# Optimization experiments

Hardware: AMD Instinct MI355X
Metric: run time of the kernel (lower is better)

The kernel has to match this reference:

```python
import jax, jax.numpy as jnp
import numpy as np

EPS = 1e-8  # F.cosine_similarity default eps


def setup_inputs() -> dict:
    key = jax.random.key(0)
    k1, k2, k3, k4 = jax.random.split(key, 4)
    Q, P, E, V = 4096, 16384, 128, 30000
    query = jax.random.randint(k1, (Q,), 0, V, dtype=jnp.int64)
    para = jax.random.randint(k2, (P,), 0, V, dtype=jnp.int64)
    que_embed = jax.random.normal(k3, (Q, E), dtype=jnp.float32)
    para_embed = jax.random.normal(k4, (P, E), dtype=jnp.float32)
    return {"query": query, "para": para, "que_embed": que_embed, "para_embed": para_embed}


def reference(query, para, que_embed, para_embed):
    # xor_matrix[i, j] = 1 if query[i] == para[j] else 0  -> [Q, P] int64
    xor_matrix = (query[:, None] == para[None, :]).astype(jnp.int64)
    # cos_matrix[i, j] = cosine_similarity(que_embed[i], para_embed[j])
    # torch semantics: dot / (max(||q||, eps) * max(||p||, eps))
    q_norm = jnp.maximum(jnp.linalg.norm(que_embed, axis=-1), EPS)   # [Q]
    p_norm = jnp.maximum(jnp.linalg.norm(para_embed, axis=-1), EPS)  # [P]
    dots = jnp.einsum('qe,pe->qp', que_embed, para_embed)            # [Q, P]
    cos_matrix = dots / (q_norm[:, None] * p_norm[None, :])
    return xor_matrix, cos_matrix
```

## Files before the change

### kernel.cpp

```cpp
#include <hip/hip_runtime.h>
#include <stdint.h>

typedef __attribute__((ext_vector_type(8))) short bf16x8;
typedef __attribute__((ext_vector_type(4))) float f32x4;

__device__ __forceinline__ uint32_t f2bf(float f) {
    uint32_t u = __builtin_bit_cast(uint32_t, f);
    u += 0x7fffu + ((u >> 16) & 1u);
    return u >> 16;
}
__device__ __forceinline__ uint32_t pack2(float a, float b) {
    return f2bf(a) | (f2bf(b) << 16);
}

__global__ __launch_bounds__(256) void prep_norms(const float* __restrict__ qe,
                                                  const float* __restrict__ pe,
                                                  float* __restrict__ rq,
                                                  float* __restrict__ rp,
                                                  int Q, int Pn) {
    int gw = (blockIdx.x * 256 + threadIdx.x) >> 6;
    int lane = threadIdx.x & 63;
    if (gw >= Q + Pn) return;
    const float* src = (gw < Q) ? (qe + (size_t)gw * 128) : (pe + (size_t)(gw - Q) * 128);
    float2 v = *(const float2*)(src + lane * 2);
    float s = v.x * v.x + v.y * v.y;
#pragma unroll
    for (int off = 32; off > 0; off >>= 1) s += __shfl_down(s, off, 64);
    if (lane == 0) {
        float r = 1.0f / fmaxf(sqrtf(s), 1e-8f);
        if (gw < Q) rq[gw] = r; else rp[gw - Q] = r;
    }
}

__global__ __launch_bounds__(256) void conv_frag(const float* __restrict__ src,
                                                 unsigned short* __restrict__ dst,
                                                 int ngroups) {
    int t = blockIdx.x * 256 + threadIdx.x;
    if (t >= ngroups * 256) return;
    int g = t >> 8, rem = t & 255;
    int c = rem >> 6, lane = rem & 63;
    int row = g * 16 + (lane & 15);
    int col = c * 32 + ((lane >> 4) << 3);
    const float* s = src + (size_t)row * 128 + col;
    float4 a0 = *(const float4*)s;
    float4 a1 = *(const float4*)(s + 4);
    uint4 pk = { pack2(a0.x, a0.y), pack2(a0.z, a0.w),
                 pack2(a1.x, a1.y), pack2(a1.z, a1.w) };
    *(uint4*)(dst + (size_t)t * 8) = pk;
}

#define PBLK 2048

__global__ __launch_bounds__(256, 4) void fused_gemm(
        const unsigned short* __restrict__ Qf, const unsigned short* __restrict__ Pf,
        const int* __restrict__ qid, const int* __restrict__ pid,
        const float* __restrict__ rq, const float* __restrict__ rp,
        float* __restrict__ oxor, float* __restrict__ ocos, int Pn) {
    __shared__ __align__(16) float scos[4 * 16 * 65];

    const int nwg = gridDim.x;
    const int chunk = nwg >> 3;
    const int bid = blockIdx.x;
    const int wg = (bid & 7) * chunk + (bid >> 3);
    const int nPc = Pn / PBLK;
    const int qg = wg / nPc;
    const int pc = wg % nPc;
    const int pblock = pc * PBLK;

    const int t = threadIdx.x;
    const int lane = t & 63;
    const int w = t >> 6;
    const int lq = lane & 15;
    const int g4 = (lane >> 4) << 2;
    const int wbase = w * (16 * 65);

    bf16x8 af[4];
    const unsigned short* abase = Qf + ((size_t)(qg * 4) * 64 + lane) * 8;
#pragma unroll
    for (int kk = 0; kk < 4; ++kk)
        af[kk] = *(const bf16x8*)(abase + kk * 512);

    const int qrow_base = qg * 16;
    const float rqv = rq[qrow_base + lq];

    for (int fl = 0; fl < PBLK / 256; ++fl) {
        const int pw = pblock + fl * 256 + w * 64;
#pragma unroll
        for (int f = 0; f < 4; ++f) {
            const int p0 = pw + f * 16;
            const unsigned short* bbase = Pf + (size_t)(p0 >> 4) * 2048 + (size_t)lane * 8;
            bf16x8 bfr[4];
#pragma unroll
            for (int kk = 0; kk < 4; ++kk)
                bfr[kk] = *(const bf16x8*)(bbase + kk * 512);
            f32x4 acc = {0.f, 0.f, 0.f, 0.f};
#pragma unroll
            for (int kk = 0; kk < 4; ++kk)
                acc = __builtin_amdgcn_mfma_f32_16x16x32_bf16(bfr[kk], af[kk], acc, 0, 0, 0);
            const float4 rpv = *(const float4*)(rp + p0 + g4);
            const int a0 = wbase + lq * 65 + f * 16 + g4;
            scos[a0 + 0] = acc[0] * rqv * rpv.x;
            scos[a0 + 1] = acc[1] * rqv * rpv.y;
            scos[a0 + 2] = acc[2] * rqv * rpv.z;
            scos[a0 + 3] = acc[3] * rqv * rpv.w;
        }
        const int pvl = pid[pw + lane];
#pragma unroll
        for (int r = 0; r < 16; ++r) {
            const int qvr = qid[qrow_base + r];
            const size_t obase = (size_t)(qrow_base + r) * Pn + pw;
            float vc = scos[wbase + r * 65 + lane];
            float vx = (qvr == pvl) ? 1.f : 0.f;
            ocos[obase + lane] = vc;
            oxor[obase + lane] = vx;
        }
    }
}

extern "C" void kernel_launch(void* const* d_in, const int* in_sizes, int n_in,
                              void* d_out, int out_size, void* d_ws, size_t ws_size,
                              hipStream_t stream) {
    const int*   qid = (const int*)d_in[0];
    const int*   pid = (const int*)d_in[1];
    const float* qe  = (const float*)d_in[2];
    const float* pe  = (const float*)d_in[3];
    const int Q  = in_sizes[0];
    const int Pn = in_sizes[1];

    unsigned short* Qf = (unsigned short*)d_ws;
    unsigned short* Pf = Qf + (size_t)Q * 128;
    float* rq = (float*)(Pf + (size_t)Pn * 128);
    float* rp = rq + Q;

    float* oxor = (float*)d_out;
    float* ocos = oxor + (size_t)Q * (size_t)Pn;

    const int qgroups = Q / 16, pgroups = Pn / 16;
    conv_frag<<<qgroups, 256, 0, stream>>>(qe, Qf, qgroups);
    conv_frag<<<pgroups, 256, 0, stream>>>(pe, Pf, pgroups);
    prep_norms<<<(Q + Pn + 3) / 4, 256, 0, stream>>>(qe, pe, rq, rp, Q, Pn);

    const int nblocks = (Q / 16) * (Pn / PBLK);
    fused_gemm<<<nblocks, 256, 0, stream>>>(Qf, Pf, qid, pid, rq, rp, oxor, ocos, Pn);
}
```

Measured before the change: 138.0 us.

## Split xor output into separate streaming kernel and vectorize cos stores

Moves the xor-matrix generation out of the GEMM into a dedicated streaming kernel that writes four floats per thread with nontemporal stores. The GEMM epilogue now writes only the cosine matrix, using 16-byte vector LDS reads and nontemporal 16-byte global stores through a padded 68-wide shared tile instead of scalar per-row stores. The aim is to raise the achieved write bandwidth, which dominates this output-bound workload. The cost is an extra kernel launch and two separate passes over the output instead of one interleaved pass.

```diff
diff --git a/kernel.cpp b/kernel.cpp
--- a/kernel.cpp
+++ b/kernel.cpp
@@ -49,14 +49,27 @@
     *(uint4*)(dst + (size_t)t * 8) = pk;
 }
 
+__global__ __launch_bounds__(256) void xor_stream(const int* __restrict__ qid,
+                                                  const int* __restrict__ pid,
+                                                  float* __restrict__ oxor,
+                                                  int Pn_log2_div4) {
+    const size_t T = (size_t)blockIdx.x * 256 + threadIdx.x;
+    const int q  = (int)(T >> Pn_log2_div4);
+    const int pi = ((int)T & ((1 << Pn_log2_div4) - 1)) << 2;
+    const int qv = qid[q];
+    const int4 pv = *(const int4*)(pid + pi);
+    f32x4 x = { pv.x == qv ? 1.f : 0.f, pv.y == qv ? 1.f : 0.f,
+                pv.z == qv ? 1.f : 0.f, pv.w == qv ? 1.f : 0.f };
+    __builtin_nontemporal_store(x, (f32x4*)(oxor + (T << 2)));
+}
+
 #define PBLK 2048
 
-__global__ __launch_bounds__(256, 4) void fused_gemm(
+__global__ __launch_bounds__(256, 4) void cos_gemm(
         const unsigned short* __restrict__ Qf, const unsigned short* __restrict__ Pf,
-        const int* __restrict__ qid, const int* __restrict__ pid,
         const float* __restrict__ rq, const float* __restrict__ rp,
-        float* __restrict__ oxor, float* __restrict__ ocos, int Pn) {
-    __shared__ __align__(16) float scos[4 * 16 * 65];
+        float* __restrict__ ocos, int Pn) {
+    __shared__ __align__(16) float scos[4][16][68];
 
     const int nwg = gridDim.x;
     const int chunk = nwg >> 3;
@@ -72,16 +85,18 @@
     const int w = t >> 6;
     const int lq = lane & 15;
     const int g4 = (lane >> 4) << 2;
-    const int wbase = w * (16 * 65);
 
     bf16x8 af[4];
-    const unsigned short* abase = Qf + ((size_t)(qg * 4) * 64 + lane) * 8;
+    const unsigned short* abase = Qf + (size_t)qg * 2048 + lane * 8;
 #pragma unroll
     for (int kk = 0; kk < 4; ++kk)
         af[kk] = *(const bf16x8*)(abase + kk * 512);
 
     const int qrow_base = qg * 16;
     const float rqv = rq[qrow_base + lq];
+
+    const int frow = lane >> 4;
+    const int fcol = (lane & 15) * 4;
 
     for (int fl = 0; fl < PBLK / 256; ++fl) {
         const int pw = pblock + fl * 256 + w * 64;
@@ -98,21 +113,16 @@
             for (int kk = 0; kk < 4; ++kk)
                 acc = __builtin_amdgcn_mfma_f32_16x16x32_bf16(bfr[kk], af[kk], acc, 0, 0, 0);
             const float4 rpv = *(const float4*)(rp + p0 + g4);
-            const int a0 = wbase + lq * 65 + f * 16 + g4;
-            scos[a0 + 0] = acc[0] * rqv * rpv.x;
-            scos[a0 + 1] = acc[1] * rqv * rpv.y;
-            scos[a0 + 2] = acc[2] * rqv * rpv.z;
-            scos[a0 + 3] = acc[3] * rqv * rpv.w;
+            f32x4 c4 = { acc[0]*rqv*rpv.x, acc[1]*rqv*rpv.y,
+                         acc[2]*rqv*rpv.z, acc[3]*rqv*rpv.w };
+            *(f32x4*)&scos[w][lq][f * 16 + g4] = c4;
         }
-        const int pvl = pid[pw + lane];
 #pragma unroll
-        for (int r = 0; r < 16; ++r) {
-            const int qvr = qid[qrow_base + r];
-            const size_t obase = (size_t)(qrow_base + r) * Pn + pw;
-            float vc = scos[wbase + r * 65 + lane];
-            float vx = (qvr == pvl) ? 1.f : 0.f;
-            ocos[obase + lane] = vc;
-            oxor[obase + lane] = vx;
+        for (int rr = 0; rr < 4; ++rr) {
+            const int row = rr * 4 + frow;
+            f32x4 vc = *(const f32x4*)&scos[w][row][fcol];
+            __builtin_nontemporal_store(vc,
+                (f32x4*)(ocos + (size_t)(qrow_base + row) * Pn + pw + fcol));
         }
     }
 }
@@ -140,6 +150,10 @@
     conv_frag<<<pgroups, 256, 0, stream>>>(pe, Pf, pgroups);
     prep_norms<<<(Q + Pn + 3) / 4, 256, 0, stream>>>(qe, pe, rq, rp, Q, Pn);
 
+    int lg = 0; while ((1 << lg) != Pn / 4) ++lg;
+    const int nxb = (int)(((size_t)Q * Pn / 4) / 256);
+    xor_stream<<<nxb, 256, 0, stream>>>(qid, pid, oxor, lg);
+
     const int nblocks = (Q / 16) * (Pn / PBLK);
-    fused_gemm<<<nblocks, 256, 0, stream>>>(Qf, Pf, qid, pid, rq, rp, oxor, ocos, Pn);
+    cos_gemm<<<nblocks, 256, 0, stream>>>(Qf, Pf, rq, rp, ocos, Pn);
 }
```

Measured after the change: 131.1 us. -5.0%, faster.
